# Optimization experiments

Measured on AMD Instinct MI355X. Metric: run time of the kernel, lower is better.

The kernel has to match this reference:

```python
import jax, jax.numpy as jnp
import numpy as np

B = 131072
IN_FEAT = 128
OUT_FEAT = 128
RANK = 32


def setup_inputs() -> dict:
    key = jax.random.key(0)
    k1, k2, k3, k4, k5 = jax.random.split(key, 5)
    inp = jax.random.normal(k1, (B, IN_FEAT), dtype=jnp.float32)
    # per-sample generated weight flattened [B, r*r], as passed to set_parameters
    gen_weight = jax.random.normal(k2, (B, RANK * RANK), dtype=jnp.float32) * 0.05
    U = jax.random.normal(k3, (IN_FEAT, RANK), dtype=jnp.float32) * (1.0 / np.sqrt(IN_FEAT))
    V = jax.random.normal(k4, (RANK, OUT_FEAT), dtype=jnp.float32) * (1.0 / np.sqrt(RANK))
    bias = jax.random.normal(k5, (OUT_FEAT,), dtype=jnp.float32) * 0.01
    return {"inp": inp, "gen_weight": gen_weight, "U": U, "V": V, "bias": bias}


def reference(inp, gen_weight, U, V, bias):
    # U_matrix projection: [B, I] -> [B, r]
    h = inp @ U
    # per-sample generated weight: [B, r*r] -> [B, r, r]
    W = gen_weight.reshape(-1, RANK, RANK)
    # (h.unsqueeze(-1) * W).sum(-2) == batched GEMV: [B, r]
    h = jnp.einsum('bi,bio->bo', h, W)
    # V_matrix projection + bias: [B, r] -> [B, O]
    out = h @ V + bias
    return out
```

## Files before the change

kernel.cpp:

```cpp
#include <hip/hip_runtime.h>


constexpr int RANK  = 32;
constexpr int BLOCK = 256;
constexpr int WPB   = BLOCK / 64;
constexpr int GRID  = 1024;
constexpr int NWAVES = GRID * WPB;

__global__ __launch_bounds__(BLOCK, 2)
void apg_linear_kernel(const float* __restrict__ inp,
                       const float* __restrict__ gw,
                       const float* __restrict__ U,
                       const float* __restrict__ V,
                       const float* __restrict__ bias,
                       float* __restrict__ out,
                       int nrows)
{
    __shared__ float4 u4s[1024];
    __shared__ float  hbuf[WPB][RANK];

    const int tid  = threadIdx.x;
    const int lane = tid & 63;
    const int wid  = tid >> 6;
    const int g    = lane >> 3;

    #pragma unroll
    for (int j = 0; j < 4; ++j)
        u4s[j * BLOCK + tid] = reinterpret_cast<const float4*>(U)[j * BLOCK + tid];
    __syncthreads();

    float2 v2[RANK];
    #pragma unroll
    for (int r = 0; r < RANK; ++r)
        v2[r] = reinterpret_cast<const float2*>(V + r * 128)[lane];
    const float2 b2 = reinterpret_cast<const float2*>(bias)[lane];

    float* hw = hbuf[wid];

    const int wave0 = blockIdx.x * WPB + wid;
    const int iters = (nrows + NWAVES - 1) / NWAVES;

    int row = wave0;
    float x0n = 0.f, x1n = 0.f;
    float4 w4n[4] = {};
    if (row < nrows) {
        x0n = inp[row * 128 + lane];
        x1n = inp[row * 128 + 64 + lane];
        const float4* wp = reinterpret_cast<const float4*>(gw) + row * 256;
        #pragma unroll
        for (int t = 0; t < 4; ++t) w4n[t] = wp[t * 64 + lane];
    }

    for (int it = 0; it < iters; ++it) {
        if (row >= nrows) break;
        const float x0 = x0n, x1 = x1n;
        float4 w4[4];
        #pragma unroll
        for (int t = 0; t < 4; ++t) w4[t] = w4n[t];

        const int nrow = row + NWAVES;
        if (it + 1 < iters && nrow < nrows) {
            x0n = inp[nrow * 128 + lane];
            x1n = inp[nrow * 128 + 64 + lane];
            const float4* wp = reinterpret_cast<const float4*>(gw) + nrow * 256;
            #pragma unroll
            for (int t = 0; t < 4; ++t) w4n[t] = wp[t * 64 + lane];
        }

        float h1a[4] = {0.f, 0.f, 0.f, 0.f};
        #pragma unroll
        for (int t = 0; t < 16; ++t) {
            const float xs = (t < 8) ? x0 : x1;
            const float xi = __shfl(xs, (t & 7) * 8 + g, 64);
            const float4 u = u4s[t * 64 + lane];
            h1a[0] = fmaf(xi, u.x, h1a[0]);
            h1a[1] = fmaf(xi, u.y, h1a[1]);
            h1a[2] = fmaf(xi, u.z, h1a[2]);
            h1a[3] = fmaf(xi, u.w, h1a[3]);
        }
        #pragma unroll
        for (int s = 8; s <= 32; s <<= 1) {
            #pragma unroll
            for (int k = 0; k < 4; ++k)
                h1a[k] += __shfl_xor(h1a[k], s, 64);
        }
        if (lane < 8)
            reinterpret_cast<float4*>(hw)[lane] =
                make_float4(h1a[0], h1a[1], h1a[2], h1a[3]);

        float h2a[4] = {0.f, 0.f, 0.f, 0.f};
        #pragma unroll
        for (int t = 0; t < 4; ++t) {
            const float hi = hw[t * 8 + g];
            h2a[0] = fmaf(hi, w4[t].x, h2a[0]);
            h2a[1] = fmaf(hi, w4[t].y, h2a[1]);
            h2a[2] = fmaf(hi, w4[t].z, h2a[2]);
            h2a[3] = fmaf(hi, w4[t].w, h2a[3]);
        }
        #pragma unroll
        for (int s = 8; s <= 32; s <<= 1) {
            #pragma unroll
            for (int k = 0; k < 4; ++k)
                h2a[k] += __shfl_xor(h2a[k], s, 64);
        }

        float o0 = b2.x, o1 = b2.y;
        #pragma unroll
        for (int r = 0; r < RANK; ++r) {
            const float h2r = __shfl(h2a[r & 3], r >> 2, 64);
            o0 = fmaf(h2r, v2[r].x, o0);
            o1 = fmaf(h2r, v2[r].y, o1);
        }
        reinterpret_cast<float2*>(out)[row * 64 + lane] = make_float2(o0, o1);

        row = nrow;
    }
}

extern "C" void kernel_launch(void* const* d_in, const int* in_sizes, int n_in,
                              void* d_out, int out_size, void* d_ws, size_t ws_size,
                              hipStream_t stream)
{
    const float* inp  = (const float*)d_in[0];
    const float* gw   = (const float*)d_in[1];
    const float* U    = (const float*)d_in[2];
    const float* V    = (const float*)d_in[3];
    const float* bias = (const float*)d_in[4];
    float* out = (float*)d_out;
    const int nrows = in_sizes[0] / 128;

    apg_linear_kernel<<<GRID, BLOCK, 0, stream>>>(inp, gw, U, V, bias, out, nrows);
}
```

Measured before the change: 140.9 us.

## Remap per-sample GEMV to one output per lane with readlane broadcasts

Each lane now owns one output column of the per-sample r×r GEMV and half the input index range, loading 16 scalar gen_weight values per row. The three-step xor-shuffle reduction shrinks to a single xor-32 step, and the 32 shuffles in the V projection become scalar readlane broadcasts. Grid size and the occupancy hint are also raised to put more waves in flight. The trade-offs are scalar instead of float4 global loads, which are still coalesced across lanes, and more registers per lane for the prefetched weights, which could strain the higher occupancy target.

Result: slower. 374.5 us (+165.9%).

```diff
diff --git a/kernel.cpp b/kernel.cpp
--- a/kernel.cpp
+++ b/kernel.cpp
@@ -4,10 +4,14 @@
 constexpr int RANK  = 32;
 constexpr int BLOCK = 256;
 constexpr int WPB   = BLOCK / 64;
-constexpr int GRID  = 1024;
+constexpr int GRID  = 2048;
 constexpr int NWAVES = GRID * WPB;
 
-__global__ __launch_bounds__(BLOCK, 2)
+__device__ __forceinline__ float bcast(float v, int srclane) {
+    return __uint_as_float(__builtin_amdgcn_readlane(__float_as_uint(v), srclane));
+}
+
+__global__ __launch_bounds__(BLOCK, 3)
 void apg_linear_kernel(const float* __restrict__ inp,
                        const float* __restrict__ gw,
                        const float* __restrict__ U,
@@ -23,6 +27,8 @@
     const int lane = tid & 63;
     const int wid  = tid >> 6;
     const int g    = lane >> 3;
+    const int o    = lane & 31;
+    const int half = lane >> 5;
 
     #pragma unroll
     for (int j = 0; j < 4; ++j)
@@ -42,29 +48,31 @@
 
     int row = wave0;
     float x0n = 0.f, x1n = 0.f;
-    float4 w4n[4] = {};
+    float wcn[16];
+    #pragma unroll
+    for (int kk = 0; kk < 16; ++kk) wcn[kk] = 0.f;
     if (row < nrows) {
         x0n = inp[row * 128 + lane];
         x1n = inp[row * 128 + 64 + lane];
-        const float4* wp = reinterpret_cast<const float4*>(gw) + row * 256;
+        const float* wb = gw + row * 1024 + half * 512 + o;
         #pragma unroll
-        for (int t = 0; t < 4; ++t) w4n[t] = wp[t * 64 + lane];
+        for (int kk = 0; kk < 16; ++kk) wcn[kk] = wb[kk * 32];
     }
 
     for (int it = 0; it < iters; ++it) {
         if (row >= nrows) break;
         const float x0 = x0n, x1 = x1n;
-        float4 w4[4];
+        float wc[16];
         #pragma unroll
-        for (int t = 0; t < 4; ++t) w4[t] = w4n[t];
+        for (int kk = 0; kk < 16; ++kk) wc[kk] = wcn[kk];
 
         const int nrow = row + NWAVES;
         if (it + 1 < iters && nrow < nrows) {
             x0n = inp[nrow * 128 + lane];
             x1n = inp[nrow * 128 + 64 + lane];
-            const float4* wp = reinterpret_cast<const float4*>(gw) + nrow * 256;
+            const float* wb = gw + nrow * 1024 + half * 512 + o;
             #pragma unroll
-            for (int t = 0; t < 4; ++t) w4n[t] = wp[t * 64 + lane];
+            for (int kk = 0; kk < 16; ++kk) wcn[kk] = wb[kk * 32];
         }
 
         float h1a[4] = {0.f, 0.f, 0.f, 0.f};
@@ -88,28 +96,23 @@
             reinterpret_cast<float4*>(hw)[lane] =
                 make_float4(h1a[0], h1a[1], h1a[2], h1a[3]);
 
-        float h2a[4] = {0.f, 0.f, 0.f, 0.f};
+        float h2 = 0.f;
         #pragma unroll
         for (int t = 0; t < 4; ++t) {
-            const float hi = hw[t * 8 + g];
-            h2a[0] = fmaf(hi, w4[t].x, h2a[0]);
-            h2a[1] = fmaf(hi, w4[t].y, h2a[1]);
-            h2a[2] = fmaf(hi, w4[t].z, h2a[2]);
-            h2a[3] = fmaf(hi, w4[t].w, h2a[3]);
+            const float4 h4 = reinterpret_cast<const float4*>(hw)[half * 4 + t];
+            h2 = fmaf(h4.x, wc[t * 4 + 0], h2);
+            h2 = fmaf(h4.y, wc[t * 4 + 1], h2);
+            h2 = fmaf(h4.z, wc[t * 4 + 2], h2);
+            h2 = fmaf(h4.w, wc[t * 4 + 3], h2);
         }
-        #pragma unroll
-        for (int s = 8; s <= 32; s <<= 1) {
-            #pragma unroll
-            for (int k = 0; k < 4; ++k)
-                h2a[k] += __shfl_xor(h2a[k], s, 64);
-        }
+        h2 += __shfl_xor(h2, 32, 64);
 
         float o0 = b2.x, o1 = b2.y;
         #pragma unroll
-        for (int r = 0; r < RANK; ++r) {
-            const float h2r = __shfl(h2a[r & 3], r >> 2, 64);
-            o0 = fmaf(h2r, v2[r].x, o0);
-            o1 = fmaf(h2r, v2[r].y, o1);
+        for (int k = 0; k < RANK; ++k) {
+            const float h2k = bcast(h2, k);
+            o0 = fmaf(h2k, v2[k].x, o0);
+            o1 = fmaf(h2k, v2[k].y, o1);
         }
         reinterpret_cast<float2*>(out)[row * 64 + lane] = make_float2(o0, o1);
 
```
